# Optimization experiments

Measured on AMD Instinct MI355X. Metric: run time of the kernel, lower is better.

Reference implementation:

```python
import jax, jax.numpy as jnp
import numpy as np


def setup_inputs() -> dict:
    key = jax.random.key(0)
    k1, k2, k3 = jax.random.split(key, 3)
    B, M, J = 4096, 64, 24  # batch, n_max_markers, n_joints
    points = jax.random.normal(k1, (B, M, 3), dtype=jnp.float32)
    weight = jax.random.uniform(k2, (B, M, J), dtype=jnp.float32)  # positive soft weights
    offset = jax.random.normal(k3, (B, M, J, 3), dtype=jnp.float32)
    return {"points": points, "weight": weight, "offset": offset}


def reference(points, weight, offset):
    # P: per-joint marker offsets (B, J, 3, M); Q: world marker positions (B, 1, 3, M)
    P = jnp.transpose(offset, (0, 2, 3, 1))
    Q = jnp.transpose(points, (0, 2, 1))[:, None]
    w = jnp.transpose(weight, (0, 2, 1))[:, :, None]  # (B, J, 1, M)

    wsum = jnp.sum(w, axis=-1)                   # (B, J, 1)
    P_ = jnp.sum(P * w, axis=-1) / wsum          # (B, J, 3) weighted centroid of offsets
    Q_ = jnp.sum(Q * w, axis=-1) / wsum          # (B, J, 3) weighted centroid of markers

    X = P - P_[..., None]                        # (B, J, 3, M)
    Y = Q - Q_[..., None]                        # (B, J, 3, M) via broadcast

    # Cross-covariance S = X @ Y^T (NOTE: original multiplies un-weighted centered coords)
    S = jnp.einsum('bjdm,bjem->bjde', X, Y)      # (B, J, 3, 3)

    U, _, Vh = jnp.linalg.svd(S)
    V = jnp.swapaxes(Vh, -1, -2)
    Ut = jnp.swapaxes(U, -1, -2)
    det = jnp.linalg.det(jnp.matmul(V, Ut))      # (B, J) reflection correction
    Ut = Ut.at[..., -1, :].multiply(det[..., None])
    R = jnp.matmul(V, Ut)                        # (B, J, 3, 3) optimal rotation
    t = Q_[..., None] - jnp.matmul(R, P_[..., None])  # (B, J, 3, 1)
    return R, t
```

## Files before the change

### kernel.cpp

```cpp
#include <hip/hip_runtime.h>


constexpr int M = 64;
constexpr int J = 24;

template<int P, int Q>
__device__ __forceinline__ void jrot(float A[4][4], float V[4][4]) {
    float apq = A[P][Q];
    float theta = (A[Q][Q] - A[P][P]) / (2.0f * apq);
    float t = 1.0f / (fabsf(theta) + sqrtf(theta * theta + 1.0f));
    t = (theta < 0.0f) ? -t : t;
    t = (apq == 0.0f) ? 0.0f : t;
    float c = 1.0f / sqrtf(t * t + 1.0f);
    float s = t * c;
#pragma unroll
    for (int k = 0; k < 4; ++k) {
        float akp = A[k][P], akq = A[k][Q];
        A[k][P] = c * akp - s * akq;
        A[k][Q] = s * akp + c * akq;
    }
#pragma unroll
    for (int k = 0; k < 4; ++k) {
        float apk = A[P][k], aqk = A[Q][k];
        A[P][k] = c * apk - s * aqk;
        A[Q][k] = s * apk + c * aqk;
        float vkp = V[k][P], vkq = V[k][Q];
        V[k][P] = c * vkp - s * vkq;
        V[k][Q] = s * vkp + c * vkq;
    }
}

__global__ __launch_bounds__(256) void kabsch_kernel(
    const float* __restrict__ points,
    const float* __restrict__ weight,
    const float* __restrict__ offset,
    float* __restrict__ out,
    int bj)
{
    int tid = blockIdx.x * blockDim.x + threadIdx.x;
    if (tid >= bj) return;
    int b = tid / J;
    int j = tid - b * J;

    const float* wq = weight + (size_t)b * M * J + j;
    const float* oq = offset + ((size_t)b * M * J + j) * 3;
    const float* pq = points + (size_t)b * M * 3;

    float W = 0.f;
    float Wo0 = 0, Wo1 = 0, Wo2 = 0, Wp0 = 0, Wp1 = 0, Wp2 = 0;
    float To0 = 0, To1 = 0, To2 = 0, Tp0 = 0, Tp1 = 0, Tp2 = 0;
    float S00 = 0, S01 = 0, S02 = 0, S10 = 0, S11 = 0, S12 = 0, S20 = 0, S21 = 0, S22 = 0;

#pragma unroll 4
    for (int m = 0; m < M; ++m) {
        float w  = wq[m * J];
        float o0 = oq[m * (J * 3) + 0];
        float o1 = oq[m * (J * 3) + 1];
        float o2 = oq[m * (J * 3) + 2];
        float p0 = pq[m * 3 + 0];
        float p1 = pq[m * 3 + 1];
        float p2 = pq[m * 3 + 2];
        W += w;
        Wo0 = fmaf(w, o0, Wo0); Wo1 = fmaf(w, o1, Wo1); Wo2 = fmaf(w, o2, Wo2);
        Wp0 = fmaf(w, p0, Wp0); Wp1 = fmaf(w, p1, Wp1); Wp2 = fmaf(w, p2, Wp2);
        To0 += o0; To1 += o1; To2 += o2;
        Tp0 += p0; Tp1 += p1; Tp2 += p2;
        S00 = fmaf(o0, p0, S00); S01 = fmaf(o0, p1, S01); S02 = fmaf(o0, p2, S02);
        S10 = fmaf(o1, p0, S10); S11 = fmaf(o1, p1, S11); S12 = fmaf(o1, p2, S12);
        S20 = fmaf(o2, p0, S20); S21 = fmaf(o2, p1, S21); S22 = fmaf(o2, p2, S22);
    }

    float inv = 1.0f / W;
    float cP0 = Wo0 * inv, cP1 = Wo1 * inv, cP2 = Wo2 * inv;
    float cQ0 = Wp0 * inv, cQ1 = Wp1 * inv, cQ2 = Wp2 * inv;

    const float fM = (float)M;
    S00 = S00 - cP0 * Tp0 - cQ0 * To0 + fM * cP0 * cQ0;
    S01 = S01 - cP0 * Tp1 - cQ1 * To0 + fM * cP0 * cQ1;
    S02 = S02 - cP0 * Tp2 - cQ2 * To0 + fM * cP0 * cQ2;
    S10 = S10 - cP1 * Tp0 - cQ0 * To1 + fM * cP1 * cQ0;
    S11 = S11 - cP1 * Tp1 - cQ1 * To1 + fM * cP1 * cQ1;
    S12 = S12 - cP1 * Tp2 - cQ2 * To1 + fM * cP1 * cQ2;
    S20 = S20 - cP2 * Tp0 - cQ0 * To2 + fM * cP2 * cQ0;
    S21 = S21 - cP2 * Tp1 - cQ1 * To2 + fM * cP2 * cQ1;
    S22 = S22 - cP2 * Tp2 - cQ2 * To2 + fM * cP2 * cQ2;

    float A[4][4], V[4][4];
    float trS = S00 + S11 + S22;
    A[0][0] = trS;
    A[0][1] = A[1][0] = S12 - S21;
    A[0][2] = A[2][0] = S20 - S02;
    A[0][3] = A[3][0] = S01 - S10;
    A[1][1] = S00 - S11 - S22;
    A[1][2] = A[2][1] = S01 + S10;
    A[1][3] = A[3][1] = S02 + S20;
    A[2][2] = -S00 + S11 - S22;
    A[2][3] = A[3][2] = S12 + S21;
    A[3][3] = -S00 - S11 + S22;

#pragma unroll
    for (int r = 0; r < 4; ++r)
#pragma unroll
        for (int c = 0; c < 4; ++c)
            V[r][c] = (r == c) ? 1.0f : 0.0f;

#pragma unroll 1
    for (int sweep = 0; sweep < 8; ++sweep) {
        jrot<0, 1>(A, V); jrot<0, 2>(A, V); jrot<0, 3>(A, V);
        jrot<1, 2>(A, V); jrot<1, 3>(A, V); jrot<2, 3>(A, V);
    }

    float best = A[0][0];
    float qw = V[0][0], qx = V[1][0], qy = V[2][0], qz = V[3][0];
#pragma unroll
    for (int i = 1; i < 4; ++i) {
        bool better = A[i][i] > best;
        best = better ? A[i][i] : best;
        qw = better ? V[0][i] : qw;
        qx = better ? V[1][i] : qx;
        qy = better ? V[2][i] : qy;
        qz = better ? V[3][i] : qz;
    }
    float nrm = 1.0f / sqrtf(qw * qw + qx * qx + qy * qy + qz * qz);
    qw *= nrm; qx *= nrm; qy *= nrm; qz *= nrm;

    float R00 = 1.f - 2.f * (qy * qy + qz * qz);
    float R01 = 2.f * (qx * qy - qw * qz);
    float R02 = 2.f * (qx * qz + qw * qy);
    float R10 = 2.f * (qx * qy + qw * qz);
    float R11 = 1.f - 2.f * (qx * qx + qz * qz);
    float R12 = 2.f * (qy * qz - qw * qx);
    float R20 = 2.f * (qx * qz - qw * qy);
    float R21 = 2.f * (qy * qz + qw * qx);
    float R22 = 1.f - 2.f * (qx * qx + qy * qy);

    float* Rout = out + (size_t)tid * 9;
    Rout[0] = R00; Rout[1] = R01; Rout[2] = R02;
    Rout[3] = R10; Rout[4] = R11; Rout[5] = R12;
    Rout[6] = R20; Rout[7] = R21; Rout[8] = R22;

    float t0 = cQ0 - (R00 * cP0 + R01 * cP1 + R02 * cP2);
    float t1 = cQ1 - (R10 * cP0 + R11 * cP1 + R12 * cP2);
    float t2 = cQ2 - (R20 * cP0 + R21 * cP1 + R22 * cP2);
    float* tout = out + (size_t)bj * 9 + (size_t)tid * 3;
    tout[0] = t0; tout[1] = t1; tout[2] = t2;
}

extern "C" void kernel_launch(void* const* d_in, const int* in_sizes, int n_in,
                              void* d_out, int out_size, void* d_ws, size_t ws_size,
                              hipStream_t stream) {
    const float* points = (const float*)d_in[0];
    const float* weight = (const float*)d_in[1];
    const float* offset = (const float*)d_in[2];
    float* out = (float*)d_out;

    int B = in_sizes[0] / (M * 3);
    int bj = B * J;
    int block = 256;
    int grid = (bj + block - 1) / block;
    kabsch_kernel<<<grid, block, 0, stream>>>(points, weight, offset, out, bj);
}
```

Measured before the change: 158.8 us.

## Split marker reduction across four threads per joint with LDS combine

Each (batch, joint) pair now uses four threads that each accumulate a strided quarter of the markers. Their 22 partial sums are combined through shared memory before one thread per pair runs the eigen solve. This quadruples the thread count and the loads in flight to hide memory latency. The cost is LDS traffic, a block barrier, and three quarters of each block idling during the solve.

```diff
diff --git a/kernel.cpp b/kernel.cpp
--- a/kernel.cpp
+++ b/kernel.cpp
@@ -3,6 +3,9 @@
 
 constexpr int M = 64;
 constexpr int J = 24;
+constexpr int KS = 4;
+constexpr int SPB = 64;
+constexpr int NACC = 22;
 
 template<int P, int Q>
 __device__ __forceinline__ void jrot(float A[4][4], float V[4][4]) {
@@ -35,59 +38,86 @@
     const float* __restrict__ weight,
     const float* __restrict__ offset,
     float* __restrict__ out,
-    int bj)
+    int bj_total)
 {
-    int tid = blockIdx.x * blockDim.x + threadIdx.x;
-    if (tid >= bj) return;
-    int b = tid / J;
-    int j = tid - b * J;
+    __shared__ float lds[NACC][SPB * KS];
 
-    const float* wq = weight + (size_t)b * M * J + j;
-    const float* oq = offset + ((size_t)b * M * J + j) * 3;
-    const float* pq = points + (size_t)b * M * 3;
+    const int t = threadIdx.x;
+    const int s = t >> 2;
+    const int k = t & 3;
+    const int bj = blockIdx.x * SPB + s;
 
-    float W = 0.f;
-    float Wo0 = 0, Wo1 = 0, Wo2 = 0, Wp0 = 0, Wp1 = 0, Wp2 = 0;
-    float To0 = 0, To1 = 0, To2 = 0, Tp0 = 0, Tp1 = 0, Tp2 = 0;
-    float S00 = 0, S01 = 0, S02 = 0, S10 = 0, S11 = 0, S12 = 0, S20 = 0, S21 = 0, S22 = 0;
+    float acc[NACC];
+#pragma unroll
+    for (int n = 0; n < NACC; ++n) acc[n] = 0.0f;
+
+    if (bj < bj_total) {
+        const int b = bj / J;
+        const int j = bj - b * J;
+        const float* wq = weight + (size_t)b * M * J + k * J + j;
+        const float* oq = offset + ((size_t)b * M * J + k * J + j) * 3;
+        const float* pq = points + (size_t)b * M * 3 + k * 3;
 
 #pragma unroll 4
-    for (int m = 0; m < M; ++m) {
-        float w  = wq[m * J];
-        float o0 = oq[m * (J * 3) + 0];
-        float o1 = oq[m * (J * 3) + 1];
-        float o2 = oq[m * (J * 3) + 2];
-        float p0 = pq[m * 3 + 0];
-        float p1 = pq[m * 3 + 1];
-        float p2 = pq[m * 3 + 2];
-        W += w;
-        Wo0 = fmaf(w, o0, Wo0); Wo1 = fmaf(w, o1, Wo1); Wo2 = fmaf(w, o2, Wo2);
-        Wp0 = fmaf(w, p0, Wp0); Wp1 = fmaf(w, p1, Wp1); Wp2 = fmaf(w, p2, Wp2);
-        To0 += o0; To1 += o1; To2 += o2;
-        Tp0 += p0; Tp1 += p1; Tp2 += p2;
-        S00 = fmaf(o0, p0, S00); S01 = fmaf(o0, p1, S01); S02 = fmaf(o0, p2, S02);
-        S10 = fmaf(o1, p0, S10); S11 = fmaf(o1, p1, S11); S12 = fmaf(o1, p2, S12);
-        S20 = fmaf(o2, p0, S20); S21 = fmaf(o2, p1, S21); S22 = fmaf(o2, p2, S22);
+        for (int i = 0; i < M / KS; ++i) {
+            float w  = wq[i * (KS * J)];
+            float o0 = oq[i * (KS * J * 3) + 0];
+            float o1 = oq[i * (KS * J * 3) + 1];
+            float o2 = oq[i * (KS * J * 3) + 2];
+            float p0 = pq[i * (KS * 3) + 0];
+            float p1 = pq[i * (KS * 3) + 1];
+            float p2 = pq[i * (KS * 3) + 2];
+            acc[0] += w;
+            acc[1] = fmaf(w, o0, acc[1]); acc[2] = fmaf(w, o1, acc[2]); acc[3] = fmaf(w, o2, acc[3]);
+            acc[4] = fmaf(w, p0, acc[4]); acc[5] = fmaf(w, p1, acc[5]); acc[6] = fmaf(w, p2, acc[6]);
+            acc[7] += o0; acc[8] += o1; acc[9] += o2;
+            acc[10] += p0; acc[11] += p1; acc[12] += p2;
+            acc[13] = fmaf(o0, p0, acc[13]); acc[14] = fmaf(o0, p1, acc[14]); acc[15] = fmaf(o0, p2, acc[15]);
+            acc[16] = fmaf(o1, p0, acc[16]); acc[17] = fmaf(o1, p1, acc[17]); acc[18] = fmaf(o1, p2, acc[18]);
+            acc[19] = fmaf(o2, p0, acc[19]); acc[20] = fmaf(o2, p1, acc[20]); acc[21] = fmaf(o2, p2, acc[21]);
+        }
     }
 
-    float inv = 1.0f / W;
-    float cP0 = Wo0 * inv, cP1 = Wo1 * inv, cP2 = Wo2 * inv;
-    float cQ0 = Wp0 * inv, cQ1 = Wp1 * inv, cQ2 = Wp2 * inv;
+#pragma unroll
+    for (int n = 0; n < NACC; ++n) lds[n][t] = acc[n];
+
+    __syncthreads();
+
+    if (t >= SPB) return;
+
+    const int bj0 = blockIdx.x * SPB + t;
+    if (bj0 >= bj_total) return;
+    const int b0 = bj0 / J;
+    const int j0 = bj0 - b0 * J;
+    (void)j0;
+
+    float T[NACC];
+#pragma unroll
+    for (int n = 0; n < NACC; ++n) {
+        float4 v = *reinterpret_cast<const float4*>(&lds[n][t * 4]);
+        T[n] = (v.x + v.y) + (v.z + v.w);
+    }
+
+    const float W = T[0];
+    const float inv = 1.0f / W;
+    const float cP0 = T[1] * inv, cP1 = T[2] * inv, cP2 = T[3] * inv;
+    const float cQ0 = T[4] * inv, cQ1 = T[5] * inv, cQ2 = T[6] * inv;
+    const float To0 = T[7], To1 = T[8], To2 = T[9];
+    const float Tp0 = T[10], Tp1 = T[11], Tp2 = T[12];
 
     const float fM = (float)M;
-    S00 = S00 - cP0 * Tp0 - cQ0 * To0 + fM * cP0 * cQ0;
-    S01 = S01 - cP0 * Tp1 - cQ1 * To0 + fM * cP0 * cQ1;
-    S02 = S02 - cP0 * Tp2 - cQ2 * To0 + fM * cP0 * cQ2;
-    S10 = S10 - cP1 * Tp0 - cQ0 * To1 + fM * cP1 * cQ0;
-    S11 = S11 - cP1 * Tp1 - cQ1 * To1 + fM * cP1 * cQ1;
-    S12 = S12 - cP1 * Tp2 - cQ2 * To1 + fM * cP1 * cQ2;
-    S20 = S20 - cP2 * Tp0 - cQ0 * To2 + fM * cP2 * cQ0;
-    S21 = S21 - cP2 * Tp1 - cQ1 * To2 + fM * cP2 * cQ1;
-    S22 = S22 - cP2 * Tp2 - cQ2 * To2 + fM * cP2 * cQ2;
+    float S00 = T[13] - cP0 * Tp0 - cQ0 * To0 + fM * cP0 * cQ0;
+    float S01 = T[14] - cP0 * Tp1 - cQ1 * To0 + fM * cP0 * cQ1;
+    float S02 = T[15] - cP0 * Tp2 - cQ2 * To0 + fM * cP0 * cQ2;
+    float S10 = T[16] - cP1 * Tp0 - cQ0 * To1 + fM * cP1 * cQ0;
+    float S11 = T[17] - cP1 * Tp1 - cQ1 * To1 + fM * cP1 * cQ1;
+    float S12 = T[18] - cP1 * Tp2 - cQ2 * To1 + fM * cP1 * cQ2;
+    float S20 = T[19] - cP2 * Tp0 - cQ0 * To2 + fM * cP2 * cQ0;
+    float S21 = T[20] - cP2 * Tp1 - cQ1 * To2 + fM * cP2 * cQ1;
+    float S22 = T[21] - cP2 * Tp2 - cQ2 * To2 + fM * cP2 * cQ2;
 
     float A[4][4], V[4][4];
-    float trS = S00 + S11 + S22;
-    A[0][0] = trS;
+    A[0][0] = S00 + S11 + S22;
     A[0][1] = A[1][0] = S12 - S21;
     A[0][2] = A[2][0] = S20 - S02;
     A[0][3] = A[3][0] = S01 - S10;
@@ -134,7 +164,7 @@
     float R21 = 2.f * (qy * qz + qw * qx);
     float R22 = 1.f - 2.f * (qx * qx + qy * qy);
 
-    float* Rout = out + (size_t)tid * 9;
+    float* Rout = out + (size_t)bj0 * 9;
     Rout[0] = R00; Rout[1] = R01; Rout[2] = R02;
     Rout[3] = R10; Rout[4] = R11; Rout[5] = R12;
     Rout[6] = R20; Rout[7] = R21; Rout[8] = R22;
@@ -142,7 +172,7 @@
     float t0 = cQ0 - (R00 * cP0 + R01 * cP1 + R02 * cP2);
     float t1 = cQ1 - (R10 * cP0 + R11 * cP1 + R12 * cP2);
     float t2 = cQ2 - (R20 * cP0 + R21 * cP1 + R22 * cP2);
-    float* tout = out + (size_t)bj * 9 + (size_t)tid * 3;
+    float* tout = out + (size_t)bj_total * 9 + (size_t)bj0 * 3;
     tout[0] = t0; tout[1] = t1; tout[2] = t2;
 }
 
@@ -155,8 +185,8 @@
     float* out = (float*)d_out;
 
     int B = in_sizes[0] / (M * 3);
-    int bj = B * J;
-    int block = 256;
-    int grid = (bj + block - 1) / block;
-    kabsch_kernel<<<grid, block, 0, stream>>>(points, weight, offset, out, bj);
+    int bj_total = B * J;
+    int block = SPB * KS;
+    int grid = (bj_total + SPB - 1) / SPB;
+    kabsch_kernel<<<grid, block, 0, stream>>>(points, weight, offset, out, bj_total);
 }
```

New measurement: 154.7 us. -2.6%, faster.
